# Kernel tuning notes

Hardware: AMD Instinct MI355X
Metric: run time of the kernel (lower is better)

The kernel has to match this reference:

```python
import jax, jax.numpy as jnp
import numpy as np

B, S, D, H = 2, 2048, 1024, 16
HD = D // H
MEAN = -1.0e9
STD = abs(MEAN) * 0.1  # min(foresight=0.5, 0.1)


def setup_inputs() -> dict:
    key = jax.random.key(0)
    ks = jax.random.split(key, 8)
    scale = 0.02
    return {
        "inputs": jax.random.normal(ks[0], (B, S, D), dtype=jnp.float32),
        "Wq": jax.random.normal(ks[1], (D, D), dtype=jnp.float32) * scale,
        "bq": jax.random.normal(ks[2], (D,), dtype=jnp.float32) * scale,
        "Wk": jax.random.normal(ks[3], (D, D), dtype=jnp.float32) * scale,
        "bk": jax.random.normal(ks[4], (D,), dtype=jnp.float32) * scale,
        "Wv": jax.random.normal(ks[5], (D, D), dtype=jnp.float32) * scale,
        "Wo": jax.random.normal(ks[6], (D, D), dtype=jnp.float32) * scale,
        "bo": jax.random.normal(ks[7], (D,), dtype=jnp.float32) * scale,
    }


def reference(inputs, Wq, bq, Wk, bk, Wv, Wo, bo):
    # projections (weights stored [in, out])
    q = (inputs @ Wq + bq).reshape(B, S, H, HD).transpose(0, 2, 1, 3)  # [B,H,S,HD]
    k = (inputs @ Wk + bk).reshape(B, S, H, HD).transpose(0, 2, 1, 3)
    v = (inputs @ Wv).reshape(B, S, H, HD).transpose(0, 2, 1, 3)

    scores = jnp.einsum("bhid,bhjd->bhij", q, k) / jnp.sqrt(jnp.float32(HD))

    # ALiBi bias as written: slopes[h] * positions[j], broadcast over query index i
    slopes = 2.0 ** (-8.0 * jnp.arange(1, H + 1, dtype=jnp.float32) / H)
    positions = jnp.arange(S, dtype=jnp.float32)
    scores = scores - slopes[None, :, None, None] * positions[None, None, None, :]

    # causal stochastic soft mask: scatter_add with identity index == elementwise add
    causal = jnp.tril(jnp.ones((S, S), dtype=jnp.float32))  # [S,S]
    soft_mask = MEAN + STD * jax.random.normal(jax.random.key(42), (B, H, S, S), dtype=jnp.float32)
    scores = scores + soft_mask * (1.0 - causal)[None, None]

    weights = jax.nn.softmax(scores, axis=-1)
    out = jnp.einsum("bhij,bhjd->bhid", weights, v)  # [B,H,S,HD]
    out = out.transpose(0, 2, 1, 3).reshape(B, S, D)
    return out @ Wo + bo
```

## Files before the change

kernel.cpp:

```cpp
#include <hip/hip_runtime.h>
#include <math.h>

#define BB 2
#define SS 2048
#define DD 1024
#define HH 16
#define HDD 64

typedef __attribute__((ext_vector_type(4))) short short4v;
typedef __attribute__((ext_vector_type(8))) short short8v;
typedef __attribute__((ext_vector_type(4))) unsigned short ushort4v;
typedef __attribute__((ext_vector_type(8))) unsigned short ushort8v;
typedef __attribute__((ext_vector_type(4))) float f32x4;

__device__ __forceinline__ unsigned short f2bf(float f) {
    union { float f; unsigned u; } v; v.f = f;
    return (unsigned short)((v.u + 0x7FFFu + ((v.u >> 16) & 1u)) >> 16);
}

__device__ __forceinline__ void gload_lds16(const void* g, void* l) {
    __builtin_amdgcn_global_load_lds(
        (const __attribute__((address_space(1))) void*)g,
        (__attribute__((address_space(3))) void*)l, 16, 0, 0);
}

__global__ __launch_bounds__(256) void convert_x(const float* __restrict__ x,
                                                 unsigned short* __restrict__ xb) {
    const size_t i = ((size_t)blockIdx.x * 256 + threadIdx.x) * 8;
    const float4 a = *(const float4*)&x[i];
    const float4 b = *(const float4*)&x[i + 4];
    ushort8v o;
    o[0] = f2bf(a.x); o[1] = f2bf(a.y); o[2] = f2bf(a.z); o[3] = f2bf(a.w);
    o[4] = f2bf(b.x); o[5] = f2bf(b.y); o[6] = f2bf(b.z); o[7] = f2bf(b.w);
    *(ushort8v*)&xb[i] = o;
}

__global__ __launch_bounds__(256) void transpose_w(
    const float* __restrict__ W0, const float* __restrict__ W1,
    const float* __restrict__ W2, const float* __restrict__ W3,
    unsigned short* __restrict__ T0, unsigned short* __restrict__ T1,
    unsigned short* __restrict__ T2, unsigned short* __restrict__ T3) {
    const int z = blockIdx.z;
    const float* W = z == 0 ? W0 : z == 1 ? W1 : z == 2 ? W2 : W3;
    unsigned short* T = z == 0 ? T0 : z == 1 ? T1 : z == 2 ? T2 : T3;
    const int k0 = blockIdx.x * 64, n0 = blockIdx.y * 64;
    const int tid = threadIdx.x;
    __shared__ unsigned short tt[64][65];
    const int rr = tid >> 4, cc = (tid & 15) * 4;
    #pragma unroll
    for (int it = 0; it < 4; ++it) {
        const int r = it * 16 + rr;
        const float4 v = *(const float4*)&W[(size_t)(k0 + r) * DD + n0 + cc];
        tt[r][cc + 0] = f2bf(v.x); tt[r][cc + 1] = f2bf(v.y);
        tt[r][cc + 2] = f2bf(v.z); tt[r][cc + 3] = f2bf(v.w);
    }
    __syncthreads();
    #pragma unroll
    for (int it = 0; it < 4; ++it) {
        const int n = it * 16 + rr;
        ushort4v o;
        o[0] = tt[cc + 0][n]; o[1] = tt[cc + 1][n];
        o[2] = tt[cc + 2][n]; o[3] = tt[cc + 3][n];
        *(ushort4v*)&T[(size_t)(n0 + n) * DD + k0 + cc] = o;
    }
}

template<int MODE, int NF>
__global__ __launch_bounds__(256) void gemm_bf16(
    const unsigned short* __restrict__ A,
    const unsigned short* __restrict__ Wt0, const unsigned short* __restrict__ Wt1,
    const unsigned short* __restrict__ Wt2,
    const float* __restrict__ bias0, const float* __restrict__ bias1,
    unsigned short* __restrict__ O0, unsigned short* __restrict__ O1,
    unsigned short* __restrict__ O2,
    float* __restrict__ Of, const float* __restrict__ biasf)
{
    constexpr int BN = NF * 32;
    const int tid = threadIdx.x;
    const int w = tid >> 6, lane = tid & 63;
    const int wm = w >> 1, wn = w & 1;
    const int c = lane & 15, g = lane >> 4;
    const int m0 = blockIdx.x * 128;

    const unsigned short* Wsel;
    int nn0, mat = 0;
    if (MODE == 0) {
        const int by = blockIdx.y;
        mat = by >> 3;
        nn0 = (by & 7) * 128;
        Wsel = mat == 0 ? Wt0 : mat == 1 ? Wt1 : Wt2;
    } else {
        nn0 = blockIdx.y * BN;
        Wsel = Wt0;
    }

    __shared__ alignas(16) unsigned short As[128 * 32];
    __shared__ alignas(16) unsigned short Bs[BN * 32];

    f32x4 acc[4][NF];
    #pragma unroll
    for (int mf = 0; mf < 4; ++mf)
        #pragma unroll
        for (int nf = 0; nf < NF; ++nf) acc[mf][nf] = f32x4{0.f, 0.f, 0.f, 0.f};

    const int lr = lane >> 2;
    const int lc8 = (lane & 3) * 8;

    for (int kt = 0; kt < DD; kt += 32) {
        #pragma unroll
        for (int i = 0; i < 2; ++i) {
            const int ii = w * 2 + i;
            gload_lds16(&A[(size_t)(m0 + ii * 16 + lr) * DD + kt + lc8], &As[ii * 512]);
        }
        if (NF == 4) {
            #pragma unroll
            for (int i = 0; i < 2; ++i) {
                const int ii = w * 2 + i;
                gload_lds16(&Wsel[(size_t)(nn0 + ii * 16 + lr) * DD + kt + lc8], &Bs[ii * 512]);
            }
        } else {
            gload_lds16(&Wsel[(size_t)(nn0 + w * 16 + lr) * DD + kt + lc8], &Bs[w * 512]);
        }
        __syncthreads();

        short8v a[4], bfr[NF];
        #pragma unroll
        for (int mf = 0; mf < 4; ++mf)
            a[mf] = *(const short8v*)&As[(wm * 64 + mf * 16 + c) * 32 + 8 * g];
        #pragma unroll
        for (int nf = 0; nf < NF; ++nf)
            bfr[nf] = *(const short8v*)&Bs[(wn * (NF * 16) + nf * 16 + c) * 32 + 8 * g];
        #pragma unroll
        for (int mf = 0; mf < 4; ++mf)
            #pragma unroll
            for (int nf = 0; nf < NF; ++nf)
                acc[mf][nf] = __builtin_amdgcn_mfma_f32_16x16x32_bf16(
                    a[mf], bfr[nf], acc[mf][nf], 0, 0, 0);
        __syncthreads();
    }

    if (MODE == 0) {
        unsigned short* Odst = mat == 0 ? O0 : mat == 1 ? O1 : O2;
        const float* bp = mat == 0 ? bias0 : mat == 1 ? bias1 : nullptr;
        #pragma unroll
        for (int nf = 0; nf < NF; ++nf) {
            const int nl = nn0 + wn * 64 + nf * 16 + c;
            const int h = nl >> 6, hd = nl & 63;
            const float bv = bp ? bp[nl] : 0.0f;
            #pragma unroll
            for (int mf = 0; mf < 4; ++mf)
                #pragma unroll
                for (int r = 0; r < 4; ++r) {
                    const int m = m0 + wm * 64 + mf * 16 + 4 * g + r;
                    const int b_ = m >> 11, s_ = m & (SS - 1);
                    Odst[(((size_t)(b_ * HH + h) * SS) + s_) * HDD + hd] =
                        f2bf(acc[mf][nf][r] + bv);
                }
        }
    } else {
        #pragma unroll
        for (int nf = 0; nf < NF; ++nf) {
            const int n = nn0 + wn * (NF * 16) + nf * 16 + c;
            const float bv = biasf[n];
            #pragma unroll
            for (int mf = 0; mf < 4; ++mf)
                #pragma unroll
                for (int r = 0; r < 4; ++r) {
                    const int m = m0 + wm * 64 + mf * 16 + 4 * g + r;
                    Of[(size_t)m * DD + n] = acc[mf][nf][r] + bv;
                }
        }
    }
}

#define LDST 76

__global__ __launch_bounds__(256) void attn_mfma_bf16(
    const unsigned short* __restrict__ Q, const unsigned short* __restrict__ K,
    const unsigned short* __restrict__ V, unsigned short* __restrict__ Out)
{
    const int lin  = blockIdx.x;
    const int xcd  = lin & 7;
    const int rest = lin >> 3;
    const int qp   = rest & 15;
    const int bh   = xcd + 8 * (rest >> 4);
    const int b = bh >> 4, h = bh & 15;
    const int tid  = threadIdx.x;
    const int w    = tid >> 6;
    const int lane = tid & 63;
    const int c    = lane & 15;
    const int g    = lane >> 4;

    __shared__ unsigned short Ks[64][LDST];
    __shared__ unsigned short Vt[64][LDST];
    __shared__ unsigned short Pw[4][16][LDST];

    const float slope = exp2f(-0.5f * (float)(h + 1));
    const float scale = 0.125f;

    const int srow = tid >> 2;
    const int scol = (tid & 3) * 16;

    #pragma unroll 1
    for (int qsel = 0; qsel < 2; ++qsel) {
        const int qt = qsel ? (SS / 64 - 1 - qp) : qp;
        const size_t baseQ = ((size_t)bh * SS + (size_t)qt * 64) * HDD;

        short8v qf[2];
        {
            const size_t qrow = baseQ + (size_t)(w * 16 + c) * HDD;
            qf[0] = *(const short8v*)&Q[qrow + 8 * g];
            qf[1] = *(const short8v*)&Q[qrow + 32 + 8 * g];
        }

        float m_[4], l_[4];
        f32x4 o_[4];
        #pragma unroll
        for (int r = 0; r < 4; ++r) { m_[r] = -3.0e38f; l_[r] = 0.0f; }
        #pragma unroll
        for (int js = 0; js < 4; ++js) o_[js] = f32x4{0.f, 0.f, 0.f, 0.f};

        for (int kt = 0; kt <= qt; ++kt) {
            __syncthreads();
            const size_t baseK = ((size_t)bh * SS + (size_t)kt * 64) * HDD;
            {
                const size_t rb = baseK + (size_t)srow * HDD + scol;
                const ushort8v k0 = *(const ushort8v*)&K[rb];
                const ushort8v k1 = *(const ushort8v*)&K[rb + 8];
                ushort4v t;
                t[0]=k0[0]; t[1]=k0[1]; t[2]=k0[2]; t[3]=k0[3];
                *(ushort4v*)&Ks[srow][scol]      = t;
                t[0]=k0[4]; t[1]=k0[5]; t[2]=k0[6]; t[3]=k0[7];
                *(ushort4v*)&Ks[srow][scol + 4]  = t;
                t[0]=k1[0]; t[1]=k1[1]; t[2]=k1[2]; t[3]=k1[3];
                *(ushort4v*)&Ks[srow][scol + 8]  = t;
                t[0]=k1[4]; t[1]=k1[5]; t[2]=k1[6]; t[3]=k1[7];
                *(ushort4v*)&Ks[srow][scol + 12] = t;
                const ushort8v v0 = *(const ushort8v*)&V[rb];
                const ushort8v v1 = *(const ushort8v*)&V[rb + 8];
                #pragma unroll
                for (int t2 = 0; t2 < 8; ++t2) {
                    Vt[scol + t2][srow]     = v0[t2];
                    Vt[scol + 8 + t2][srow] = v1[t2];
                }
            }
            __syncthreads();

            f32x4 acc[4];
            #pragma unroll
            for (int js = 0; js < 4; ++js) {
                f32x4 a = {0.f, 0.f, 0.f, 0.f};
                const int krow = js * 16 + c;
                #pragma unroll
                for (int ks = 0; ks < 2; ++ks) {
                    short4v lo = *(const short4v*)&Ks[krow][32 * ks + 8 * g];
                    short4v hi = *(const short4v*)&Ks[krow][32 * ks + 8 * g + 4];
                    short8v kf = {lo[0], lo[1], lo[2], lo[3], hi[0], hi[1], hi[2], hi[3]};
                    a = __builtin_amdgcn_mfma_f32_16x16x32_bf16(qf[ks], kf, a, 0, 0, 0);
                }
                acc[js] = a;
            }

            float s[4][4];
            const int jb = kt * 64 + c;
            const bool diag = (kt == qt);
            const int iloc = w * 16 + 4 * g;
            #pragma unroll
            for (int js = 0; js < 4; ++js) {
                const float ab = slope * (float)(jb + 16 * js);
                #pragma unroll
                for (int r = 0; r < 4; ++r) {
                    float val = acc[js][r] * scale - ab;
                    if (diag && (16 * js + c) > (iloc + r)) val = -3.0e38f;
                    s[js][r] = val;
                }
            }

            float corr[4];
            #pragma unroll
            for (int r = 0; r < 4; ++r) {
                float mr = fmaxf(fmaxf(s[0][r], s[1][r]), fmaxf(s[2][r], s[3][r]));
                #pragma unroll
                for (int off = 8; off; off >>= 1)
                    mr = fmaxf(mr, __shfl_xor(mr, off, 64));
                const float mn = fmaxf(m_[r], mr);
                corr[r] = __expf(m_[r] - mn);
                m_[r] = mn;
            }
            float rs[4] = {0.f, 0.f, 0.f, 0.f};
            #pragma unroll
            for (int js = 0; js < 4; ++js) {
                #pragma unroll
                for (int r = 0; r < 4; ++r) {
                    const float p = __expf(s[js][r] - m_[r]);
                    rs[r] += p;
                    Pw[w][4 * g + r][js * 16 + c] = f2bf(p);
                }
            }
            #pragma unroll
            for (int r = 0; r < 4; ++r) {
                #pragma unroll
                for (int off = 8; off; off >>= 1)
                    rs[r] += __shfl_xor(rs[r], off, 64);
                l_[r] = l_[r] * corr[r] + rs[r];
            }
            #pragma unroll
            for (int js = 0; js < 4; ++js) {
                #pragma unroll
                for (int r = 0; r < 4; ++r) o_[js][r] *= corr[r];
            }

            asm volatile("s_waitcnt lgkmcnt(0)" ::: "memory");

            short8v pf[2];
            #pragma unroll
            for (int ks = 0; ks < 2; ++ks) {
                short4v lo = *(const short4v*)&Pw[w][c][32 * ks + 8 * g];
                short4v hi = *(const short4v*)&Pw[w][c][32 * ks + 8 * g + 4];
                short8v f = {lo[0], lo[1], lo[2], lo[3], hi[0], hi[1], hi[2], hi[3]};
                pf[ks] = f;
            }
            #pragma unroll
            for (int js = 0; js < 4; ++js) {
                const int vrow = js * 16 + c;
                #pragma unroll
                for (int ks = 0; ks < 2; ++ks) {
                    short4v lo = *(const short4v*)&Vt[vrow][32 * ks + 8 * g];
                    short4v hi = *(const short4v*)&Vt[vrow][32 * ks + 8 * g + 4];
                    short8v vf = {lo[0], lo[1], lo[2], lo[3], hi[0], hi[1], hi[2], hi[3]};
                    o_[js] = __builtin_amdgcn_mfma_f32_16x16x32_bf16(pf[ks], vf, o_[js], 0, 0, 0);
                }
            }
        }

        float inv[4];
        #pragma unroll
        for (int r = 0; r < 4; ++r) inv[r] = 1.0f / l_[r];
        const size_t baseO = ((size_t)b * SS + (size_t)qt * 64 + w * 16) * DD + h * HDD;
        #pragma unroll
        for (int js = 0; js < 4; ++js) {
            #pragma unroll
            for (int r = 0; r < 4; ++r) {
                Out[baseO + (size_t)(4 * g + r) * DD + js * 16 + c] =
                    f2bf(o_[js][r] * inv[r]);
            }
        }
    }
}

extern "C" void kernel_launch(void* const* d_in, const int* in_sizes, int n_in,
                              void* d_out, int out_size, void* d_ws, size_t ws_size,
                              hipStream_t stream) {
    const float* x  = (const float*)d_in[0];
    const float* Wq = (const float*)d_in[1];
    const float* bq = (const float*)d_in[2];
    const float* Wk = (const float*)d_in[3];
    const float* bk = (const float*)d_in[4];
    const float* Wv = (const float*)d_in[5];
    const float* Wo = (const float*)d_in[6];
    const float* bo = (const float*)d_in[7];

    unsigned short* ws = (unsigned short*)d_ws;
    unsigned short* xb    = ws;
    unsigned short* Wqt   = xb + 4194304;
    unsigned short* Wkt   = Wqt + 1048576;
    unsigned short* Wvt   = Wkt + 1048576;
    unsigned short* Wot   = Wvt + 1048576;
    unsigned short* Qb    = Wot + 1048576;
    unsigned short* Kb    = Qb + 4194304;
    unsigned short* Vb    = Kb + 4194304;
    unsigned short* attnb = Vb + 4194304;

    convert_x<<<2048, 256, 0, stream>>>(x, xb);
    transpose_w<<<dim3(16, 16, 4), 256, 0, stream>>>(Wq, Wk, Wv, Wo,
                                                     Wqt, Wkt, Wvt, Wot);

    gemm_bf16<0, 4><<<dim3(32, 24), 256, 0, stream>>>(
        xb, Wqt, Wkt, Wvt, bq, bk, Qb, Kb, Vb, nullptr, nullptr);

    attn_mfma_bf16<<<512, 256, 0, stream>>>(Qb, Kb, Vb, attnb);

    gemm_bf16<1, 2><<<dim3(32, 16), 256, 0, stream>>>(
        attnb, Wot, nullptr, nullptr, nullptr, nullptr,
        nullptr, nullptr, nullptr, (float*)d_out, bo);
}
```

Before: 234.1 us.

## Launch one query tile per block, longest first, with exp2 and deferred rescaling

Replaces the paired light/heavy query-tile scheme (512 blocks doing two tiles each) with 1024 blocks of one tile each, ordered so the tiles with the most key blocks go first. Folds log2(e) into the scale and slope so exp2f can replace __expf. Skips rescaling of the running max and output when no row's max grows by more than a threshold, wave-uniformly. Also changes the LDS row padding from 76 to 77. Deferred rescaling risks fp32 overflow headroom, and the odd 77-element padding misaligns the short4 LDS accesses.

```diff
diff --git a/kernel.cpp b/kernel.cpp
--- a/kernel.cpp
+++ b/kernel.cpp
@@ -173,7 +173,7 @@
     }
 }
 
-#define LDST 76
+#define LDST 77
 
 __global__ __launch_bounds__(256) void attn_mfma_bf16(
     const unsigned short* __restrict__ Q, const unsigned short* __restrict__ K,
@@ -182,8 +182,8 @@
     const int lin  = blockIdx.x;
     const int xcd  = lin & 7;
     const int rest = lin >> 3;
-    const int qp   = rest & 15;
-    const int bh   = xcd + 8 * (rest >> 4);
+    const int qt   = 31 - (rest & 31);
+    const int bh   = xcd + 8 * (rest >> 5);
     const int b = bh >> 4, h = bh & 15;
     const int tid  = threadIdx.x;
     const int w    = tid >> 6;
@@ -195,155 +195,170 @@
     __shared__ unsigned short Vt[64][LDST];
     __shared__ unsigned short Pw[4][16][LDST];
 
-    const float slope = exp2f(-0.5f * (float)(h + 1));
-    const float scale = 0.125f;
+    const float LOG2E = 1.44269504f;
+    const float slope = exp2f(-0.5f * (float)(h + 1)) * LOG2E;
+    const float scale = 0.125f * LOG2E;
 
     const int srow = tid >> 2;
     const int scol = (tid & 3) * 16;
 
-    #pragma unroll 1
-    for (int qsel = 0; qsel < 2; ++qsel) {
-        const int qt = qsel ? (SS / 64 - 1 - qp) : qp;
-        const size_t baseQ = ((size_t)bh * SS + (size_t)qt * 64) * HDD;
-
-        short8v qf[2];
+    const size_t baseQ = ((size_t)bh * SS + (size_t)qt * 64) * HDD;
+
+    short8v qf[2];
+    {
+        const size_t qrow = baseQ + (size_t)(w * 16 + c) * HDD;
+        qf[0] = *(const short8v*)&Q[qrow + 8 * g];
+        qf[1] = *(const short8v*)&Q[qrow + 32 + 8 * g];
+    }
+
+    float m_[4], l_[4];
+    f32x4 o_[4];
+    #pragma unroll
+    for (int r = 0; r < 4; ++r) { m_[r] = -3.0e38f; l_[r] = 0.0f; }
+    #pragma unroll
+    for (int js = 0; js < 4; ++js) o_[js] = f32x4{0.f, 0.f, 0.f, 0.f};
+
+    for (int kt = 0; kt <= qt; ++kt) {
+        __syncthreads();
+        const size_t baseK = ((size_t)bh * SS + (size_t)kt * 64) * HDD;
         {
-            const size_t qrow = baseQ + (size_t)(w * 16 + c) * HDD;
-            qf[0] = *(const short8v*)&Q[qrow + 8 * g];
-            qf[1] = *(const short8v*)&Q[qrow + 32 + 8 * g];
-        }
-
-        float m_[4], l_[4];
-        f32x4 o_[4];
-        #pragma unroll
-        for (int r = 0; r < 4; ++r) { m_[r] = -3.0e38f; l_[r] = 0.0f; }
-        #pragma unroll
-        for (int js = 0; js < 4; ++js) o_[js] = f32x4{0.f, 0.f, 0.f, 0.f};
-
-        for (int kt = 0; kt <= qt; ++kt) {
-            __syncthreads();
-            const size_t baseK = ((size_t)bh * SS + (size_t)kt * 64) * HDD;
-            {
-                const size_t rb = baseK + (size_t)srow * HDD + scol;
-                const ushort8v k0 = *(const ushort8v*)&K[rb];
-                const ushort8v k1 = *(const ushort8v*)&K[rb + 8];
-                ushort4v t;
-                t[0]=k0[0]; t[1]=k0[1]; t[2]=k0[2]; t[3]=k0[3];
-                *(ushort4v*)&Ks[srow][scol]      = t;
-                t[0]=k0[4]; t[1]=k0[5]; t[2]=k0[6]; t[3]=k0[7];
-                *(ushort4v*)&Ks[srow][scol + 4]  = t;
-                t[0]=k1[0]; t[1]=k1[1]; t[2]=k1[2]; t[3]=k1[3];
-                *(ushort4v*)&Ks[srow][scol + 8]  = t;
-                t[0]=k1[4]; t[1]=k1[5]; t[2]=k1[6]; t[3]=k1[7];
-                *(ushort4v*)&Ks[srow][scol + 12] = t;
-                const ushort8v v0 = *(const ushort8v*)&V[rb];
-                const ushort8v v1 = *(const ushort8v*)&V[rb + 8];
-                #pragma unroll
-                for (int t2 = 0; t2 < 8; ++t2) {
-                    Vt[scol + t2][srow]     = v0[t2];
-                    Vt[scol + 8 + t2][srow] = v1[t2];
-                }
-            }
-            __syncthreads();
-
-            f32x4 acc[4];
-            #pragma unroll
-            for (int js = 0; js < 4; ++js) {
-                f32x4 a = {0.f, 0.f, 0.f, 0.f};
-                const int krow = js * 16 + c;
-                #pragma unroll
-                for (int ks = 0; ks < 2; ++ks) {
-                    short4v lo = *(const short4v*)&Ks[krow][32 * ks + 8 * g];
-                    short4v hi = *(const short4v*)&Ks[krow][32 * ks + 8 * g + 4];
-                    short8v kf = {lo[0], lo[1], lo[2], lo[3], hi[0], hi[1], hi[2], hi[3]};
-                    a = __builtin_amdgcn_mfma_f32_16x16x32_bf16(qf[ks], kf, a, 0, 0, 0);
-                }
-                acc[js] = a;
-            }
-
-            float s[4][4];
-            const int jb = kt * 64 + c;
-            const bool diag = (kt == qt);
-            const int iloc = w * 16 + 4 * g;
-            #pragma unroll
-            for (int js = 0; js < 4; ++js) {
-                const float ab = slope * (float)(jb + 16 * js);
-                #pragma unroll
-                for (int r = 0; r < 4; ++r) {
-                    float val = acc[js][r] * scale - ab;
-                    if (diag && (16 * js + c) > (iloc + r)) val = -3.0e38f;
-                    s[js][r] = val;
-                }
-            }
-
-            float corr[4];
+            const size_t rb = baseK + (size_t)srow * HDD + scol;
+            const ushort8v k0 = *(const ushort8v*)&K[rb];
+            const ushort8v k1 = *(const ushort8v*)&K[rb + 8];
+            ushort4v t;
+            t[0]=k0[0]; t[1]=k0[1]; t[2]=k0[2]; t[3]=k0[3];
+            *(ushort4v*)&Ks[srow][scol]      = t;
+            t[0]=k0[4]; t[1]=k0[5]; t[2]=k0[6]; t[3]=k0[7];
+            *(ushort4v*)&Ks[srow][scol + 4]  = t;
+            t[0]=k1[0]; t[1]=k1[1]; t[2]=k1[2]; t[3]=k1[3];
+            *(ushort4v*)&Ks[srow][scol + 8]  = t;
+            t[0]=k1[4]; t[1]=k1[5]; t[2]=k1[6]; t[3]=k1[7];
+            *(ushort4v*)&Ks[srow][scol + 12] = t;
+            const ushort8v v0 = *(const ushort8v*)&V[rb];
+            const ushort8v v1 = *(const ushort8v*)&V[rb + 8];
+            #pragma unroll
+            for (int t2 = 0; t2 < 8; ++t2) {
+                Vt[scol + t2][srow]     = v0[t2];
+                Vt[scol + 8 + t2][srow] = v1[t2];
+            }
+        }
+        __syncthreads();
+
+        f32x4 acc[4];
+        #pragma unroll
+        for (int js = 0; js < 4; ++js) {
+            f32x4 a = {0.f, 0.f, 0.f, 0.f};
+            const int krow = js * 16 + c;
+            #pragma unroll
+            for (int ks = 0; ks < 2; ++ks) {
+                short4v lo = *(const short4v*)&Ks[krow][32 * ks + 8 * g];
+                short4v hi = *(const short4v*)&Ks[krow][32 * ks + 8 * g + 4];
+                short8v kf = {lo[0], lo[1], lo[2], lo[3], hi[0], hi[1], hi[2], hi[3]};
+                a = __builtin_amdgcn_mfma_f32_16x16x32_bf16(qf[ks], kf, a, 0, 0, 0);
+            }
+            acc[js] = a;
+        }
+
+        float s[4][4];
+        const int jb = kt * 64 + c;
+        const bool diag = (kt == qt);
+        const int iloc = w * 16 + 4 * g;
+        #pragma unroll
+        for (int js = 0; js < 4; ++js) {
+            const float ab = slope * (float)(jb + 16 * js);
             #pragma unroll
             for (int r = 0; r < 4; ++r) {
-                float mr = fmaxf(fmaxf(s[0][r], s[1][r]), fmaxf(s[2][r], s[3][r]));
-                #pragma unroll
-                for (int off = 8; off; off >>= 1)
-                    mr = fmaxf(mr, __shfl_xor(mr, off, 64));
-                const float mn = fmaxf(m_[r], mr);
-                corr[r] = __expf(m_[r] - mn);
+                float val = acc[js][r] * scale - ab;
+                if (diag && (16 * js + c) > (iloc + r)) val = -1.0e30f;
+                s[js][r] = val;
+            }
+        }
+
+        float mr[4];
+        #pragma unroll
+        for (int r = 0; r < 4; ++r) {
+            float v = fmaxf(fmaxf(s[0][r], s[1][r]), fmaxf(s[2][r], s[3][r]));
+            #pragma unroll
+            for (int off = 8; off; off >>= 1)
+                v = fmaxf(v, __shfl_xor(v, off, 64));
+            mr[r] = v;
+        }
+        float dmax = mr[0] - m_[0];
+        #pragma unroll
+        for (int r = 1; r < 4; ++r) dmax = fmaxf(dmax, mr[r] - m_[r]);
+        const bool defer = __all(dmax <= 11.5f);
+
+        float corr[4];
+        if (!defer) {
+            #pragma unroll
+            for (int r = 0; r < 4; ++r) {
+                const float mn = fmaxf(m_[r], mr[r]);
+                corr[r] = exp2f(m_[r] - mn);
                 m_[r] = mn;
             }
-            float rs[4] = {0.f, 0.f, 0.f, 0.f};
-            #pragma unroll
-            for (int js = 0; js < 4; ++js) {
-                #pragma unroll
-                for (int r = 0; r < 4; ++r) {
-                    const float p = __expf(s[js][r] - m_[r]);
-                    rs[r] += p;
-                    Pw[w][4 * g + r][js * 16 + c] = f2bf(p);
-                }
-            }
+        }
+
+        float rs[4] = {0.f, 0.f, 0.f, 0.f};
+        #pragma unroll
+        for (int js = 0; js < 4; ++js) {
             #pragma unroll
             for (int r = 0; r < 4; ++r) {
-                #pragma unroll
-                for (int off = 8; off; off >>= 1)
-                    rs[r] += __shfl_xor(rs[r], off, 64);
-                l_[r] = l_[r] * corr[r] + rs[r];
-            }
-            #pragma unroll
-            for (int js = 0; js < 4; ++js) {
+                const float p = exp2f(s[js][r] - m_[r]);
+                rs[r] += p;
+                Pw[w][4 * g + r][js * 16 + c] = f2bf(p);
+            }
+        }
+        #pragma unroll
+        for (int r = 0; r < 4; ++r) {
+            #pragma unroll
+            for (int off = 8; off; off >>= 1)
+                rs[r] += __shfl_xor(rs[r], off, 64);
+        }
+        if (defer) {
+            #pragma unroll
+            for (int r = 0; r < 4; ++r) l_[r] += rs[r];
+        } else {
+            #pragma unroll
+            for (int r = 0; r < 4; ++r) l_[r] = l_[r] * corr[r] + rs[r];
+            #pragma unroll
+            for (int js = 0; js < 4; ++js)
                 #pragma unroll
                 for (int r = 0; r < 4; ++r) o_[js][r] *= corr[r];
-            }
-
-            asm volatile("s_waitcnt lgkmcnt(0)" ::: "memory");
-
-            short8v pf[2];
+        }
+
+        asm volatile("s_waitcnt lgkmcnt(0)" ::: "memory");
+
+        short8v pf[2];
+        #pragma unroll
+        for (int ks = 0; ks < 2; ++ks) {
+            short4v lo = *(const short4v*)&Pw[w][c][32 * ks + 8 * g];
+            short4v hi = *(const short4v*)&Pw[w][c][32 * ks + 8 * g + 4];
+            short8v f = {lo[0], lo[1], lo[2], lo[3], hi[0], hi[1], hi[2], hi[3]};
+            pf[ks] = f;
+        }
+        #pragma unroll
+        for (int js = 0; js < 4; ++js) {
+            const int vrow = js * 16 + c;
             #pragma unroll
             for (int ks = 0; ks < 2; ++ks) {
-                short4v lo = *(const short4v*)&Pw[w][c][32 * ks + 8 * g];
-                short4v hi = *(const short4v*)&Pw[w][c][32 * ks + 8 * g + 4];
-                short8v f = {lo[0], lo[1], lo[2], lo[3], hi[0], hi[1], hi[2], hi[3]};
-                pf[ks] = f;
-            }
-            #pragma unroll
-            for (int js = 0; js < 4; ++js) {
-                const int vrow = js * 16 + c;
-                #pragma unroll
-                for (int ks = 0; ks < 2; ++ks) {
-                    short4v lo = *(const short4v*)&Vt[vrow][32 * ks + 8 * g];
-                    short4v hi = *(const short4v*)&Vt[vrow][32 * ks + 8 * g + 4];
-                    short8v vf = {lo[0], lo[1], lo[2], lo[3], hi[0], hi[1], hi[2], hi[3]};
-                    o_[js] = __builtin_amdgcn_mfma_f32_16x16x32_bf16(pf[ks], vf, o_[js], 0, 0, 0);
-                }
-            }
-        }
-
-        float inv[4];
-        #pragma unroll
-        for (int r = 0; r < 4; ++r) inv[r] = 1.0f / l_[r];
-        const size_t baseO = ((size_t)b * SS + (size_t)qt * 64 + w * 16) * DD + h * HDD;
-        #pragma unroll
-        for (int js = 0; js < 4; ++js) {
-            #pragma unroll
-            for (int r = 0; r < 4; ++r) {
-                Out[baseO + (size_t)(4 * g + r) * DD + js * 16 + c] =
-                    f2bf(o_[js][r] * inv[r]);
-            }
+                short4v lo = *(const short4v*)&Vt[vrow][32 * ks + 8 * g];
+                short4v hi = *(const short4v*)&Vt[vrow][32 * ks + 8 * g + 4];
+                short8v vf = {lo[0], lo[1], lo[2], lo[3], hi[0], hi[1], hi[2], hi[3]};
+                o_[js] = __builtin_amdgcn_mfma_f32_16x16x32_bf16(pf[ks], vf, o_[js], 0, 0, 0);
+            }
+        }
+    }
+
+    float inv[4];
+    #pragma unroll
+    for (int r = 0; r < 4; ++r) inv[r] = 1.0f / l_[r];
+    const size_t baseO = ((size_t)b * SS + (size_t)qt * 64 + w * 16) * DD + h * HDD;
+    #pragma unroll
+    for (int js = 0; js < 4; ++js) {
+        #pragma unroll
+        for (int r = 0; r < 4; ++r) {
+            Out[baseO + (size_t)(4 * g + r) * DD + js * 16 + c] =
+                f2bf(o_[js][r] * inv[r]);
         }
     }
 }
@@ -378,7 +393,7 @@
     gemm_bf16<0, 4><<<dim3(32, 24), 256, 0, stream>>>(
         xb, Wqt, Wkt, Wvt, bq, bk, Qb, Kb, Vb, nullptr, nullptr);
 
-    attn_mfma_bf16<<<512, 256, 0, stream>>>(Qb, Kb, Vb, attnb);
+    attn_mfma_bf16<<<1024, 256, 0, stream>>>(Qb, Kb, Vb, attnb);
 
     gemm_bf16<1, 2><<<dim3(32, 16), 256, 0, stream>>>(
         attnb, Wot, nullptr, nullptr, nullptr, nullptr,
```

Measured after the change: 498.0 us. 2.13x slower.
